# Optimization experiments

Hardware: AMD Instinct MI355X
Metric: run time of the kernel (lower is better)

Reference implementation:

```python
import jax, jax.numpy as jnp
import numpy as np

MEM, KD, VD, H, TEMP = 4096, 512, 512, 8, 1.0
B, N, BW = 4, 1024, 1024


def setup_inputs() -> dict:
    key = jax.random.key(0)
    ks = jax.random.split(key, 9)
    s = 0.02
    return {
        "queries": jax.random.normal(ks[0], (B, N, KD), jnp.float32),
        "write_keys": jax.random.normal(ks[1], (BW, KD), jnp.float32),
        "write_values": jax.random.normal(ks[2], (BW, VD), jnp.float32),
        "mem_keys": jax.random.normal(ks[3], (MEM, KD), jnp.float32),
        "mem_values": jax.random.normal(ks[4], (MEM, VD), jnp.float32),
        "Wq": jax.random.normal(ks[5], (KD, KD * H), jnp.float32) * s,
        "bq": jnp.zeros((KD * H,), jnp.float32),
        "Wvp": jax.random.normal(ks[6], (H * VD, VD), jnp.float32) * s,
        "bvp": jnp.zeros((VD,), jnp.float32),
        "Wg": jax.random.normal(ks[7], (KD + VD, KD), jnp.float32) * s,
        "bg": jnp.zeros((KD,), jnp.float32),
    }


def _read(queries, mem_keys, mem_values, Wq, bq, Wvp, bvp):
    b, n, _ = queries.shape
    q = queries @ Wq + bq                       # [b, n, H*KD]
    q = q.reshape(b, n, H, KD).transpose(0, 2, 1, 3)  # [b, h, n, d]
    # keys/values are shared across batch & heads: contract directly, no repeat
    scores = jnp.einsum('bhnd,md->bhnm', q, mem_keys) / (KD ** 0.5) / TEMP
    attn = jax.nn.softmax(scores, axis=-1)
    rv = jnp.einsum('bhnm,md->bhnd', attn, mem_values)  # [b, h, n, VD]
    rv = rv.transpose(0, 2, 1, 3).reshape(b, n, H * VD)
    return rv @ Wvp + bvp                        # [b, n, VD]


def _write(write_keys, write_values, mem_keys, mem_values, Wg, bg):
    eps = 1e-8
    kn = write_keys / jnp.maximum(jnp.linalg.norm(write_keys, axis=-1, keepdims=True), eps)
    mn = mem_keys / jnp.maximum(jnp.linalg.norm(mem_keys, axis=-1, keepdims=True), eps)
    idx = jnp.argmax(kn @ mn.T, axis=1)          # [BW] fixed against original keys

    def step(carry, inp):
        K, V = carry
        k, v, i = inp
        combined = jnp.concatenate([k, V[i]], axis=-1)   # reads current values
        gate = jax.nn.sigmoid(combined @ Wg + bg)        # [KD]
        K = K.at[i].set(gate * k + (1.0 - gate) * K[i])
        V = V.at[i].set(gate * v + (1.0 - gate) * V[i])
        return (K, V), None

    (nk, nv), _ = jax.lax.scan(step, (mem_keys, mem_values), (write_keys, write_values, idx))
    return nk, nv


def reference(queries, write_keys, write_values, mem_keys, mem_values, Wq, bq, Wvp, bvp, Wg, bg):
    read_out = _read(queries, mem_keys, mem_values, Wq, bq, Wvp, bvp)
    new_keys, new_values = _write(write_keys, write_values, mem_keys, mem_values, Wg, bg)
    return read_out, new_keys, new_values
```

## Files before the change

### kernel.cpp

```cpp
#include <hip/hip_runtime.h>
#include <cstdint>
#include <cstddef>

typedef __attribute__((ext_vector_type(8))) short short8;
typedef __attribute__((ext_vector_type(4))) float f32x4;
typedef unsigned char u8;
typedef unsigned short u16;
typedef unsigned int u32;
typedef unsigned long long u64;

__device__ __forceinline__ u16 f2bf(float f) {
    u32 u = __float_as_uint(f);
    u = (u + 0x7FFFu + ((u >> 16) & 1u)) >> 16;
    return (u16)u;
}
__device__ __forceinline__ float bf2f(u16 h) {
    u32 u = ((u32)h) << 16;
    return __uint_as_float(u);
}
__device__ __forceinline__ u8 f2fp8(float f) {
    return (u8)(__builtin_amdgcn_cvt_pk_fp8_f32(f, f, 0, false) & 0xFF);
}

__global__ void cast_bf16_kernel(const float* __restrict__ src, u16* __restrict__ dst) {
    int i = blockIdx.x * 256 + threadIdx.x;
    float4 v = *((const float4*)src + i);
    ushort4 r;
    r.x = f2bf(v.x); r.y = f2bf(v.y); r.z = f2bf(v.z); r.w = f2bf(v.w);
    *((ushort4*)dst + i) = r;
}

__global__ void split_bf16_kernel(const float* __restrict__ src,
                                  u16* __restrict__ hi, u16* __restrict__ lo) {
    int i = blockIdx.x * 256 + threadIdx.x;
    float4 v = *((const float4*)src + i);
    ushort4 h, l;
    h.x = f2bf(v.x); l.x = f2bf(v.x - bf2f(h.x));
    h.y = f2bf(v.y); l.y = f2bf(v.y - bf2f(h.y));
    h.z = f2bf(v.z); l.z = f2bf(v.z - bf2f(h.z));
    h.w = f2bf(v.w); l.w = f2bf(v.w - bf2f(h.w));
    *((ushort4*)hi + i) = h;
    *((ushort4*)lo + i) = l;
}

__global__ void cast_transpose_kernel(const float* __restrict__ src, u16* __restrict__ dst,
                                      int R, int C) {
    __shared__ float tile[32][33];
    int tx = threadIdx.x & 31, ty = threadIdx.x >> 5;
    int c0 = blockIdx.x * 32, r0 = blockIdx.y * 32;
#pragma unroll
    for (int j = 0; j < 4; j++)
        tile[ty + 8 * j][tx] = src[(size_t)(r0 + ty + 8 * j) * C + c0 + tx];
    __syncthreads();
#pragma unroll
    for (int j = 0; j < 4; j++)
        dst[(size_t)(c0 + ty + 8 * j) * R + r0 + tx] = f2bf(tile[tx][ty + 8 * j]);
}

__global__ void cast_transpose_fp8_kernel(const float* __restrict__ src, u8* __restrict__ dst,
                                          int R, int C) {
    __shared__ float tile[32][33];
    int tx = threadIdx.x & 31, ty = threadIdx.x >> 5;
    int c0 = blockIdx.x * 32, r0 = blockIdx.y * 32;
#pragma unroll
    for (int j = 0; j < 4; j++)
        tile[ty + 8 * j][tx] = src[(size_t)(r0 + ty + 8 * j) * C + c0 + tx];
    __syncthreads();
#pragma unroll
    for (int j = 0; j < 4; j++)
        dst[(size_t)(c0 + ty + 8 * j) * R + r0 + tx] = f2fp8(tile[tx][ty + 8 * j]);
}

__global__ __launch_bounds__(256) void key_prep_kernel(const float* __restrict__ mk,
                                                       u16* __restrict__ mn_hi,
                                                       u16* __restrict__ mn_lo,
                                                       u16* __restrict__ Kb) {
    int row = blockIdx.x, tid = threadIdx.x;
    const float* src = mk + (size_t)row * 512;
    float x0 = src[tid], x1 = src[tid + 256];
    float ss = x0 * x0 + x1 * x1;
#pragma unroll
    for (int m = 1; m < 64; m <<= 1) ss += __shfl_xor(ss, m);
    __shared__ float sred[4];
    if ((tid & 63) == 0) sred[tid >> 6] = ss;
    __syncthreads();
    float tot = sred[0] + sred[1] + sred[2] + sred[3];
    float inv = 1.0f / fmaxf(sqrtf(tot), 1e-8f);
    float n0 = x0 * inv, n1 = x1 * inv;
    u16 h0 = f2bf(n0), h1 = f2bf(n1);
    mn_hi[(size_t)row * 512 + tid] = h0;
    mn_hi[(size_t)row * 512 + tid + 256] = h1;
    mn_lo[(size_t)row * 512 + tid] = f2bf(n0 - bf2f(h0));
    mn_lo[(size_t)row * 512 + tid + 256] = f2bf(n1 - bf2f(h1));
    Kb[(size_t)row * 512 + tid] = f2bf(x0);
    Kb[(size_t)row * 512 + tid + 256] = f2bf(x1);
}

template <int BN, int EPI>
__global__ __launch_bounds__(256, 2) void gemm_bt_kernel(const u16* __restrict__ A,
                                                         const u16* __restrict__ Bt,
                                                         const float* __restrict__ bias,
                                                         void* __restrict__ Cout,
                                                         int M, int N, int K) {
    constexpr int NT = BN / 32;
    __shared__ __align__(16) u16 A_lds[128 * 40];
    __shared__ __align__(16) u16 B_lds[BN * 40];
    int tid = threadIdx.x;
    int w = tid >> 6, lane = tid & 63, l15 = lane & 15, quad = lane >> 4;
    int wm = w >> 1, wn = w & 1;
    int n0 = blockIdx.x * BN, m0 = blockIdx.y * 128;

    f32x4 acc[4][NT];
#pragma unroll
    for (int i = 0; i < 4; i++)
#pragma unroll
        for (int j = 0; j < NT; j++) acc[i][j] = (f32x4)(0.0f);

    for (int kt = 0; kt < K; kt += 32) {
        __syncthreads();
#pragma unroll
        for (int i = 0; i < 2; i++) {
            int c = i * 256 + tid;
            int r = c >> 2, col = c & 3;
            *(uint4*)&A_lds[r * 40 + col * 8] =
                *(const uint4*)&A[(size_t)(m0 + r) * K + kt + col * 8];
        }
#pragma unroll
        for (int i = 0; i < BN / 64; i++) {
            int c = i * 256 + tid;
            int r = c >> 2, col = c & 3;
            *(uint4*)&B_lds[r * 40 + col * 8] =
                *(const uint4*)&Bt[(size_t)(n0 + r) * K + kt + col * 8];
        }
        __syncthreads();
        short8 af[4], bf[NT];
#pragma unroll
        for (int mt = 0; mt < 4; mt++)
            af[mt] = *(const short8*)&A_lds[(wm * 64 + mt * 16 + l15) * 40 + quad * 8];
#pragma unroll
        for (int nt = 0; nt < NT; nt++)
            bf[nt] = *(const short8*)&B_lds[(wn * (BN / 2) + nt * 16 + l15) * 40 + quad * 8];
#pragma unroll
        for (int mt = 0; mt < 4; mt++)
#pragma unroll
            for (int nt = 0; nt < NT; nt++)
                acc[mt][nt] = __builtin_amdgcn_mfma_f32_16x16x32_bf16(af[mt], bf[nt], acc[mt][nt], 0, 0, 0);
    }

#pragma unroll
    for (int nt = 0; nt < NT; nt++) {
        int col = n0 + wn * (BN / 2) + nt * 16 + l15;
        float bs = bias[col];
#pragma unroll
        for (int mt = 0; mt < 4; mt++) {
            int row = m0 + wm * 64 + mt * 16 + quad * 4;
#pragma unroll
            for (int r = 0; r < 4; r++) {
                float v = acc[mt][nt][r] + bs;
                if (EPI == 0) {
                    ((float*)Cout)[(size_t)(row + r) * N + col] = v;
                } else {
                    int rr = row + r;
                    int bi = rr >> 10, ni = rr & 1023;
                    int h = col >> 9, d = col & 511;
                    ((u16*)Cout)[(((size_t)((bi * 8 + h)) * 1024 + ni)) * 512 + d] = f2bf(v);
                }
            }
        }
    }
}

__global__ __launch_bounds__(256, 2) void s_exp_gemm_kernel(const u16* __restrict__ A,
                                                            const u16* __restrict__ Bt,
                                                            u8* __restrict__ P,
                                                            float* __restrict__ denom) {
    __shared__ __align__(16) u16 A_lds[128 * 40];
    __shared__ __align__(16) u16 B_lds[128 * 40];
    int tid = threadIdx.x;
    int w = tid >> 6, lane = tid & 63, l15 = lane & 15, quad = lane >> 4;
    int wm = w >> 1, wn = w & 1;
    int n0 = blockIdx.x * 128, m0 = blockIdx.y * 128;

    f32x4 acc[4][4];
#pragma unroll
    for (int i = 0; i < 4; i++)
#pragma unroll
        for (int j = 0; j < 4; j++) acc[i][j] = (f32x4)(0.0f);

    for (int kt = 0; kt < 512; kt += 32) {
        __syncthreads();
#pragma unroll
        for (int i = 0; i < 2; i++) {
            int c = i * 256 + tid;
            int r = c >> 2, col = c & 3;
            *(uint4*)&A_lds[r * 40 + col * 8] =
                *(const uint4*)&A[(size_t)(m0 + r) * 512 + kt + col * 8];
            *(uint4*)&B_lds[r * 40 + col * 8] =
                *(const uint4*)&Bt[(size_t)(n0 + r) * 512 + kt + col * 8];
        }
        __syncthreads();
        short8 af[4], bf[4];
#pragma unroll
        for (int mt = 0; mt < 4; mt++)
            af[mt] = *(const short8*)&A_lds[(wm * 64 + mt * 16 + l15) * 40 + quad * 8];
#pragma unroll
        for (int nt = 0; nt < 4; nt++)
            bf[nt] = *(const short8*)&B_lds[(wn * 64 + nt * 16 + l15) * 40 + quad * 8];
#pragma unroll
        for (int mt = 0; mt < 4; mt++)
#pragma unroll
            for (int nt = 0; nt < 4; nt++)
                acc[mt][nt] = __builtin_amdgcn_mfma_f32_16x16x32_bf16(af[mt], bf[nt], acc[mt][nt], 0, 0, 0);
    }

    const float sc = 0.06375871826463886f;
#pragma unroll
    for (int mt = 0; mt < 4; mt++) {
#pragma unroll
        for (int r = 0; r < 4; r++) {
            int row = m0 + wm * 64 + mt * 16 + quad * 4 + r;
            float rs = 0.f;
#pragma unroll
            for (int nt = 0; nt < 4; nt++) {
                float p = exp2f(acc[mt][nt][r] * sc);
                rs += p;
                float pnb = __shfl_xor(p, 1);
                float plo = (l15 & 1) ? pnb : p;
                float phi = (l15 & 1) ? p : pnb;
                u32 pk2 = (u32)__builtin_amdgcn_cvt_pk_fp8_f32(plo, phi, 0, false) & 0xFFFFu;
                u32 oth = __shfl_xor(pk2, 2);
                u32 dw = (l15 & 2) ? (oth | (pk2 << 16)) : (pk2 | (oth << 16));
                if ((l15 & 3) == 0) {
                    int col = n0 + wn * 64 + nt * 16 + l15;
                    *(u32*)&P[(size_t)row * 4096 + col] = dw;
                }
            }
            rs += __shfl_xor(rs, 1); rs += __shfl_xor(rs, 2);
            rs += __shfl_xor(rs, 4); rs += __shfl_xor(rs, 8);
            if (l15 == 0) atomicAdd(&denom[row], rs);
        }
    }
}

__global__ __launch_bounds__(256, 2) void pv_gemm_kernel(const u8* __restrict__ A,
                                                         const u8* __restrict__ Bt,
                                                         const float* __restrict__ denom,
                                                         u16* __restrict__ rv,
                                                         int bh0) {
    __shared__ __align__(16) u8 A_lds[128 * 72];
    __shared__ __align__(16) u8 B_lds[128 * 72];
    int tid = threadIdx.x;
    int w = tid >> 6, lane = tid & 63, l15 = lane & 15, quad = lane >> 4;
    int wm = w >> 1, wn = w & 1;
    int m0 = blockIdx.x * 128, n0 = blockIdx.y * 128;

    f32x4 acc[4][4];
#pragma unroll
    for (int i = 0; i < 4; i++)
#pragma unroll
        for (int j = 0; j < 4; j++) acc[i][j] = (f32x4)(0.0f);

    for (int kt = 0; kt < 4096; kt += 64) {
        __syncthreads();
#pragma unroll
        for (int i = 0; i < 2; i++) {
            int c = i * 256 + tid;
            int r = c >> 2, seg = c & 3;
            *(uint4*)&A_lds[r * 72 + seg * 16] =
                *(const uint4*)&A[(size_t)(m0 + r) * 4096 + kt + seg * 16];
            *(uint4*)&B_lds[r * 72 + seg * 16] =
                *(const uint4*)&Bt[(size_t)(n0 + r) * 4096 + kt + seg * 16];
        }
        __syncthreads();
#pragma unroll
        for (int ks = 0; ks < 2; ks++) {
            long af[4], bf[4];
#pragma unroll
            for (int mt = 0; mt < 4; mt++)
                af[mt] = *(const long*)&A_lds[(wm * 64 + mt * 16 + l15) * 72 + ks * 32 + quad * 8];
#pragma unroll
            for (int nt = 0; nt < 4; nt++)
                bf[nt] = *(const long*)&B_lds[(wn * 64 + nt * 16 + l15) * 72 + ks * 32 + quad * 8];
#pragma unroll
            for (int mt = 0; mt < 4; mt++)
#pragma unroll
                for (int nt = 0; nt < 4; nt++)
                    acc[mt][nt] = __builtin_amdgcn_mfma_f32_16x16x32_fp8_fp8(af[mt], bf[nt], acc[mt][nt], 0, 0, 0);
        }
    }

#pragma unroll
    for (int mt = 0; mt < 4; mt++) {
#pragma unroll
        for (int r = 0; r < 4; r++) {
            int lr = m0 + wm * 64 + mt * 16 + quad * 4 + r;
            int gr = bh0 * 1024 + lr;
            float inv = 1.0f / denom[lr];
            int b = gr >> 13, h = (gr >> 10) & 7, n = gr & 1023;
            size_t base = ((size_t)(b * 1024 + n)) * 4096 + h * 512;
#pragma unroll
            for (int nt = 0; nt < 4; nt++) {
                int col = n0 + wn * 64 + nt * 16 + l15;
                float o = acc[mt][nt][r] * inv;
                float onb = __shfl_xor(o, 1);
                u16 blo = f2bf((l15 & 1) ? onb : o);
                u16 bhi = f2bf((l15 & 1) ? o : onb);
                u32 dw = (u32)blo | ((u32)bhi << 16);
                if (!(l15 & 1)) *(u32*)&rv[base + col] = dw;
            }
        }
    }
}

__global__ __launch_bounds__(256, 2) void sims_mfma_kernel(const u16* __restrict__ Ah,
                                                           const u16* __restrict__ Al,
                                                           const u16* __restrict__ Bh,
                                                           const u16* __restrict__ Bl,
                                                           u64* __restrict__ amax) {
    __shared__ __align__(16) u16 Ah_lds[128 * 40];
    __shared__ __align__(16) u16 Al_lds[128 * 40];
    __shared__ __align__(16) u16 Bh_lds[128 * 40];
    __shared__ __align__(16) u16 Bl_lds[128 * 40];
    int tid = threadIdx.x;
    int w = tid >> 6, lane = tid & 63, l15 = lane & 15, quad = lane >> 4;
    int wm = w >> 1, wn = w & 1;
    int n0 = blockIdx.x * 128, m0 = blockIdx.y * 128;

    f32x4 acc[4][4];
#pragma unroll
    for (int i = 0; i < 4; i++)
#pragma unroll
        for (int j = 0; j < 4; j++) acc[i][j] = (f32x4)(0.0f);

    for (int kt = 0; kt < 512; kt += 32) {
        __syncthreads();
#pragma unroll
        for (int i = 0; i < 2; i++) {
            int c = i * 256 + tid;
            int r = c >> 2, col = c & 3;
            size_t ga = (size_t)(m0 + r) * 512 + kt + col * 8;
            size_t gb = (size_t)(n0 + r) * 512 + kt + col * 8;
            *(uint4*)&Ah_lds[r * 40 + col * 8] = *(const uint4*)&Ah[ga];
            *(uint4*)&Al_lds[r * 40 + col * 8] = *(const uint4*)&Al[ga];
            *(uint4*)&Bh_lds[r * 40 + col * 8] = *(const uint4*)&Bh[gb];
            *(uint4*)&Bl_lds[r * 40 + col * 8] = *(const uint4*)&Bl[gb];
        }
        __syncthreads();
        short8 afh[4], afl[4], bfh[4], bfl[4];
#pragma unroll
        for (int mt = 0; mt < 4; mt++) {
            int off = (wm * 64 + mt * 16 + l15) * 40 + quad * 8;
            afh[mt] = *(const short8*)&Ah_lds[off];
            afl[mt] = *(const short8*)&Al_lds[off];
        }
#pragma unroll
        for (int nt = 0; nt < 4; nt++) {
            int off = (wn * 64 + nt * 16 + l15) * 40 + quad * 8;
            bfh[nt] = *(const short8*)&Bh_lds[off];
            bfl[nt] = *(const short8*)&Bl_lds[off];
        }
#pragma unroll
        for (int mt = 0; mt < 4; mt++)
#pragma unroll
            for (int nt = 0; nt < 4; nt++) {
                acc[mt][nt] = __builtin_amdgcn_mfma_f32_16x16x32_bf16(afh[mt], bfh[nt], acc[mt][nt], 0, 0, 0);
                acc[mt][nt] = __builtin_amdgcn_mfma_f32_16x16x32_bf16(afh[mt], bfl[nt], acc[mt][nt], 0, 0, 0);
                acc[mt][nt] = __builtin_amdgcn_mfma_f32_16x16x32_bf16(afl[mt], bfh[nt], acc[mt][nt], 0, 0, 0);
            }
    }

#pragma unroll
    for (int mt = 0; mt < 4; mt++) {
#pragma unroll
        for (int r = 0; r < 4; r++) {
            int row = m0 + wm * 64 + mt * 16 + quad * 4 + r;
            u64 best = 0;
#pragma unroll
            for (int nt = 0; nt < 4; nt++) {
                int col = n0 + wn * 64 + nt * 16 + l15;
                u32 bb = __float_as_uint(acc[mt][nt][r]);
                bb = (bb & 0x80000000u) ? ~bb : (bb | 0x80000000u);
                u64 key = ((u64)bb << 32) | (u32)(4095 - col);
                best = best > key ? best : key;
            }
            u64 o;
            o = __shfl_xor(best, 1); best = best > o ? best : o;
            o = __shfl_xor(best, 2); best = best > o ? best : o;
            o = __shfl_xor(best, 4); best = best > o ? best : o;
            o = __shfl_xor(best, 8); best = best > o ? best : o;
            if (l15 == 0) atomicMax(&amax[row], best);
        }
    }
}

__global__ __launch_bounds__(64) void chains_build_kernel(const u64* __restrict__ amax,
                                                          int* __restrict__ idx,
                                                          int* __restrict__ nxt,
                                                          int* __restrict__ heads,
                                                          int* __restrict__ count) {
    __shared__ int sidx[1024];
    int tid = threadIdx.x;
    for (int j = tid; j < 1024; j += 64)
        sidx[j] = 4095 - (int)(u32)(amax[j] & 0xFFFFFFFFull);
    __syncthreads();
    int i = blockIdx.x * 64 + tid;
    int my = sidx[i];
    idx[i] = my;
    int nx = -1;
    for (int j = i + 1; j < 1024; j++)
        if (sidx[j] == my) { nx = j; break; }
    nxt[i] = nx;
    bool head = true;
    for (int j = 0; j < i; j++)
        if (sidx[j] == my) { head = false; break; }
    if (head) {
        int p = atomicAdd(count, 1);
        heads[p] = i;
    }
}

__global__ __launch_bounds__(256) void g1_gemm_kernel(const float* __restrict__ wk,
                                                      const float* __restrict__ Wg,
                                                      const float* __restrict__ bg,
                                                      float* __restrict__ G1) {
    __shared__ float wkl[8][512];
    int tid = threadIdx.x;
    int i0 = blockIdx.x * 8;
    for (int i = tid; i < 8 * 512; i += 256) wkl[i >> 9][i & 511] = wk[(size_t)i0 * 512 + i];
    __syncthreads();
    float a0[8], a1[8];
#pragma unroll
    for (int i = 0; i < 8; i++) { a0[i] = 0.f; a1[i] = 0.f; }
    for (int c = 0; c < 512; c++) {
        float w0 = Wg[(size_t)c * 512 + tid];
        float w1 = Wg[(size_t)c * 512 + tid + 256];
#pragma unroll
        for (int ii = 0; ii < 8; ii++) {
            float s = wkl[ii][c];
            a0[ii] += s * w0; a1[ii] += s * w1;
        }
    }
    float b0 = bg[tid], b1 = bg[tid + 256];
#pragma unroll
    for (int ii = 0; ii < 8; ii++) {
        G1[(size_t)(i0 + ii) * 512 + tid] = a0[ii] + b0;
        G1[(size_t)(i0 + ii) * 512 + tid + 256] = a1[ii] + b1;
    }
}

__global__ __launch_bounds__(256) void chain_apply_kernel(const int* __restrict__ heads,
                                                          const int* __restrict__ count,
                                                          const int* __restrict__ idx,
                                                          const int* __restrict__ nxt,
                                                          const float* __restrict__ G1,
                                                          const float* __restrict__ Wg,
                                                          const float* __restrict__ wk,
                                                          const float* __restrict__ wv,
                                                          const float* __restrict__ mk,
                                                          const float* __restrict__ mv,
                                                          float* __restrict__ outK,
                                                          float* __restrict__ outV) {
    int b = blockIdx.x;
    if (b >= *count) return;
    int i = heads[b];
    int s = idx[i];
    int tid = threadIdx.x;
    __shared__ float V[512];
    V[tid] = mv[(size_t)s * 512 + tid];
    V[tid + 256] = mv[(size_t)s * 512 + tid + 256];
    float k0 = mk[(size_t)s * 512 + tid], k1 = mk[(size_t)s * 512 + tid + 256];
    __syncthreads();
    while (i >= 0) {
        float a0 = G1[(size_t)i * 512 + tid], a1 = G1[(size_t)i * 512 + tid + 256];
        for (int c = 0; c < 512; c++) {
            float vc = V[c];
            a0 += vc * Wg[(size_t)(512 + c) * 512 + tid];
            a1 += vc * Wg[(size_t)(512 + c) * 512 + tid + 256];
        }
        float g0 = 1.f / (1.f + __expf(-a0));
        float g1 = 1.f / (1.f + __expf(-a1));
        __syncthreads();
        k0 = g0 * wk[(size_t)i * 512 + tid] + (1.f - g0) * k0;
        k1 = g1 * wk[(size_t)i * 512 + tid + 256] + (1.f - g1) * k1;
        V[tid] = g0 * wv[(size_t)i * 512 + tid] + (1.f - g0) * V[tid];
        V[tid + 256] = g1 * wv[(size_t)i * 512 + tid + 256] + (1.f - g1) * V[tid + 256];
        __syncthreads();
        i = nxt[i];
    }
    outK[(size_t)s * 512 + tid] = k0;
    outK[(size_t)s * 512 + tid + 256] = k1;
    outV[(size_t)s * 512 + tid] = V[tid];
    outV[(size_t)s * 512 + tid + 256] = V[tid + 256];
}

extern "C" void kernel_launch(void* const* d_in, const int* in_sizes, int n_in,
                              void* d_out, int out_size, void* d_ws, size_t ws_size,
                              hipStream_t stream) {
    const float* queries = (const float*)d_in[0];
    const float* wkeys   = (const float*)d_in[1];
    const float* wvals   = (const float*)d_in[2];
    const float* mkeys   = (const float*)d_in[3];
    const float* mvals   = (const float*)d_in[4];
    const float* Wq      = (const float*)d_in[5];
    const float* bq      = (const float*)d_in[6];
    const float* Wvp     = (const float*)d_in[7];
    const float* bvp     = (const float*)d_in[8];
    const float* Wg      = (const float*)d_in[9];
    const float* bg      = (const float*)d_in[10];

    float* out_read = (float*)d_out;
    float* out_k = out_read + (size_t)4 * 1024 * 512;
    float* out_v = out_k + (size_t)4096 * 512;

    char* ws = (char*)d_ws;
    const size_t MB = 1024 * 1024;
    u16* Qbf  = (u16*)(ws);
    u16* WqT  = (u16*)(ws + 4 * MB);
    u16* Qatt = (u16*)(ws + 8 * MB);
    u16* Kb   = (u16*)(ws + 40 * MB);
    u8*  Vt8  = (u8*)(ws + 44 * MB);
    u16* rv   = (u16*)(ws + 48 * MB);
    u16* WvpT = (u16*)(ws + 80 * MB);
    u16* mn_hi = (u16*)(ws + 84 * MB);
    u16* mn_lo = (u16*)(ws + 88 * MB);
    float* G1  = (float*)(ws + 92 * MB);
    u16* wk_hi = (u16*)(ws + 94 * MB);
    u16* wk_lo = (u16*)(ws + 95 * MB);
    u64* amax   = (u64*)(ws);
    int* count  = (int*)(ws + 8192);
    int* idx    = (int*)(ws + 8192 + 256);
    int* nxt    = (int*)(ws + 8192 + 256 + 4096);
    int* heads  = (int*)(ws + 8192 + 256 + 8192);
    float* denom = (float*)(ws + 32 * 1024);
    u8* P = (u8*)(ws + 84 * MB);
    (void)in_sizes; (void)n_in; (void)out_size;

    size_t avail = (ws_size > 84 * MB) ? ws_size - 84 * MB : 0;
    int G = 2;
    for (int g = 32; g >= 2; g >>= 1)
        if ((size_t)g * 4 * MB <= avail) { G = g; break; }

    hipMemcpyAsync(out_k, mkeys, (size_t)4096 * 512 * 4, hipMemcpyDeviceToDevice, stream);
    hipMemcpyAsync(out_v, mvals, (size_t)4096 * 512 * 4, hipMemcpyDeviceToDevice, stream);

    cast_bf16_kernel<<<2048, 256, 0, stream>>>(queries, Qbf);
    cast_transpose_kernel<<<dim3(4096 / 32, 512 / 32), 256, 0, stream>>>(Wq, WqT, 512, 4096);
    cast_transpose_kernel<<<dim3(512 / 32, 4096 / 32), 256, 0, stream>>>(Wvp, WvpT, 4096, 512);
    cast_transpose_fp8_kernel<<<dim3(512 / 32, 4096 / 32), 256, 0, stream>>>(mvals, Vt8, 4096, 512);
    key_prep_kernel<<<4096, 256, 0, stream>>>(mkeys, mn_hi, mn_lo, Kb);
    split_bf16_kernel<<<512, 256, 0, stream>>>(wkeys, wk_hi, wk_lo);

    gemm_bt_kernel<128, 1><<<dim3(32, 32), 256, 0, stream>>>(Qbf, WqT, bq, (void*)Qatt, 4096, 4096, 512);

    hipMemsetAsync(ws, 0, 8192 + 256, stream);
    hipMemsetAsync(denom, 0, 32768 * 4, stream);
    sims_mfma_kernel<<<dim3(32, 8), 256, 0, stream>>>(wk_hi, wk_lo, mn_hi, mn_lo, amax);
    chains_build_kernel<<<16, 64, 0, stream>>>(amax, idx, nxt, heads, count);
    g1_gemm_kernel<<<128, 256, 0, stream>>>(wkeys, Wg, bg, G1);
    chain_apply_kernel<<<1024, 256, 0, stream>>>(heads, count, idx, nxt, G1, Wg,
                                                 wkeys, wvals, mkeys, mvals, out_k, out_v);

    for (int bh0 = 0; bh0 < 32; bh0 += G) {
        const u16* Achunk = Qatt + (size_t)bh0 * 1024 * 512;
        float* dchunk = denom + bh0 * 1024;
        s_exp_gemm_kernel<<<dim3(32, G * 8), 256, 0, stream>>>(Achunk, Kb, P, dchunk);
        pv_gemm_kernel<<<dim3(G * 8, 4), 256, 0, stream>>>(P, Vt8, dchunk, rv, bh0);
    }

    gemm_bt_kernel<64, 0><<<dim3(8, 32), 256, 0, stream>>>(rv, WvpT, bvp, (void*)out_read, 4096, 512, 4096);
}
```

Before: 825.7 us.

## Use direct global-to-LDS loads with XOR-swizzled unpadded tiles in GEMM kernels

Replaces register-staged global loads followed by LDS stores with global_load_lds direct transfers in all four MFMA GEMM kernels. Because direct LDS loads write contiguous 16-byte chunks per lane, the padded row stride is dropped and an XOR swizzle on the chunk index is applied when loading and when reading fragments, to avoid bank conflicts. This is meant to cut VGPR pressure and instruction count in the load phase. The loops stay single-buffered, so load latency still is not overlapped, and the swizzle has to match the fragment read pattern exactly.

```diff
diff --git a/kernel.cpp b/kernel.cpp
--- a/kernel.cpp
+++ b/kernel.cpp
@@ -20,6 +20,11 @@
 }
 __device__ __forceinline__ u8 f2fp8(float f) {
     return (u8)(__builtin_amdgcn_cvt_pk_fp8_f32(f, f, 0, false) & 0xFF);
+}
+
+__device__ __forceinline__ void gl_lds16(const void* g, void* l) {
+    __builtin_amdgcn_global_load_lds((const __attribute__((address_space(1))) void*)g,
+                                     (__attribute__((address_space(3))) void*)l, 16, 0, 0);
 }
 
 __global__ void cast_bf16_kernel(const float* __restrict__ src, u16* __restrict__ dst) {
@@ -103,12 +108,13 @@
                                                          void* __restrict__ Cout,
                                                          int M, int N, int K) {
     constexpr int NT = BN / 32;
-    __shared__ __align__(16) u16 A_lds[128 * 40];
-    __shared__ __align__(16) u16 B_lds[BN * 40];
+    __shared__ __align__(16) u16 A_lds[128 * 32];
+    __shared__ __align__(16) u16 B_lds[BN * 32];
     int tid = threadIdx.x;
     int w = tid >> 6, lane = tid & 63, l15 = lane & 15, quad = lane >> 4;
     int wm = w >> 1, wn = w & 1;
     int n0 = blockIdx.x * BN, m0 = blockIdx.y * 128;
+    int sa = (l15 >> 1) & 3;
 
     f32x4 acc[4][NT];
 #pragma unroll
@@ -121,25 +127,23 @@
 #pragma unroll
         for (int i = 0; i < 2; i++) {
             int c = i * 256 + tid;
-            int r = c >> 2, col = c & 3;
-            *(uint4*)&A_lds[r * 40 + col * 8] =
-                *(const uint4*)&A[(size_t)(m0 + r) * K + kt + col * 8];
+            int r = c >> 2, s = (c & 3) ^ ((r >> 1) & 3);
+            gl_lds16(&A[(size_t)(m0 + r) * K + kt + s * 8], &A_lds[c * 8]);
         }
 #pragma unroll
         for (int i = 0; i < BN / 64; i++) {
             int c = i * 256 + tid;
-            int r = c >> 2, col = c & 3;
-            *(uint4*)&B_lds[r * 40 + col * 8] =
-                *(const uint4*)&Bt[(size_t)(n0 + r) * K + kt + col * 8];
+            int r = c >> 2, s = (c & 3) ^ ((r >> 1) & 3);
+            gl_lds16(&Bt[(size_t)(n0 + r) * K + kt + s * 8], &B_lds[c * 8]);
         }
         __syncthreads();
         short8 af[4], bf[NT];
 #pragma unroll
         for (int mt = 0; mt < 4; mt++)
-            af[mt] = *(const short8*)&A_lds[(wm * 64 + mt * 16 + l15) * 40 + quad * 8];
+            af[mt] = *(const short8*)&A_lds[(wm * 64 + mt * 16 + l15) * 32 + (quad ^ sa) * 8];
 #pragma unroll
         for (int nt = 0; nt < NT; nt++)
-            bf[nt] = *(const short8*)&B_lds[(wn * (BN / 2) + nt * 16 + l15) * 40 + quad * 8];
+            bf[nt] = *(const short8*)&B_lds[(wn * (BN / 2) + nt * 16 + l15) * 32 + (quad ^ sa) * 8];
 #pragma unroll
         for (int mt = 0; mt < 4; mt++)
 #pragma unroll
@@ -174,12 +178,13 @@
                                                             const u16* __restrict__ Bt,
                                                             u8* __restrict__ P,
                                                             float* __restrict__ denom) {
-    __shared__ __align__(16) u16 A_lds[128 * 40];
-    __shared__ __align__(16) u16 B_lds[128 * 40];
+    __shared__ __align__(16) u16 A_lds[128 * 32];
+    __shared__ __align__(16) u16 B_lds[128 * 32];
     int tid = threadIdx.x;
     int w = tid >> 6, lane = tid & 63, l15 = lane & 15, quad = lane >> 4;
     int wm = w >> 1, wn = w & 1;
     int n0 = blockIdx.x * 128, m0 = blockIdx.y * 128;
+    int sa = (l15 >> 1) & 3;
 
     f32x4 acc[4][4];
 #pragma unroll
@@ -192,20 +197,18 @@
 #pragma unroll
         for (int i = 0; i < 2; i++) {
             int c = i * 256 + tid;
-            int r = c >> 2, col = c & 3;
-            *(uint4*)&A_lds[r * 40 + col * 8] =
-                *(const uint4*)&A[(size_t)(m0 + r) * 512 + kt + col * 8];
-            *(uint4*)&B_lds[r * 40 + col * 8] =
-                *(const uint4*)&Bt[(size_t)(n0 + r) * 512 + kt + col * 8];
+            int r = c >> 2, s = (c & 3) ^ ((r >> 1) & 3);
+            gl_lds16(&A[(size_t)(m0 + r) * 512 + kt + s * 8], &A_lds[c * 8]);
+            gl_lds16(&Bt[(size_t)(n0 + r) * 512 + kt + s * 8], &B_lds[c * 8]);
         }
         __syncthreads();
         short8 af[4], bf[4];
 #pragma unroll
         for (int mt = 0; mt < 4; mt++)
-            af[mt] = *(const short8*)&A_lds[(wm * 64 + mt * 16 + l15) * 40 + quad * 8];
+            af[mt] = *(const short8*)&A_lds[(wm * 64 + mt * 16 + l15) * 32 + (quad ^ sa) * 8];
 #pragma unroll
         for (int nt = 0; nt < 4; nt++)
-            bf[nt] = *(const short8*)&B_lds[(wn * 64 + nt * 16 + l15) * 40 + quad * 8];
+            bf[nt] = *(const short8*)&B_lds[(wn * 64 + nt * 16 + l15) * 32 + (quad ^ sa) * 8];
 #pragma unroll
         for (int mt = 0; mt < 4; mt++)
 #pragma unroll
@@ -247,12 +250,13 @@
                                                          const float* __restrict__ denom,
                                                          u16* __restrict__ rv,
                                                          int bh0) {
-    __shared__ __align__(16) u8 A_lds[128 * 72];
-    __shared__ __align__(16) u8 B_lds[128 * 72];
+    __shared__ __align__(16) u8 A_lds[128 * 64];
+    __shared__ __align__(16) u8 B_lds[128 * 64];
     int tid = threadIdx.x;
     int w = tid >> 6, lane = tid & 63, l15 = lane & 15, quad = lane >> 4;
     int wm = w >> 1, wn = w & 1;
     int m0 = blockIdx.x * 128, n0 = blockIdx.y * 128;
+    int sa = (l15 >> 1) & 3;
 
     f32x4 acc[4][4];
 #pragma unroll
@@ -265,22 +269,24 @@
 #pragma unroll
         for (int i = 0; i < 2; i++) {
             int c = i * 256 + tid;
-            int r = c >> 2, seg = c & 3;
-            *(uint4*)&A_lds[r * 72 + seg * 16] =
-                *(const uint4*)&A[(size_t)(m0 + r) * 4096 + kt + seg * 16];
-            *(uint4*)&B_lds[r * 72 + seg * 16] =
-                *(const uint4*)&Bt[(size_t)(n0 + r) * 4096 + kt + seg * 16];
+            int r = c >> 2, s = (c & 3) ^ ((r >> 1) & 3);
+            gl_lds16(&A[(size_t)(m0 + r) * 4096 + kt + s * 16], &A_lds[c * 16]);
+            gl_lds16(&Bt[(size_t)(n0 + r) * 4096 + kt + s * 16], &B_lds[c * 16]);
         }
         __syncthreads();
 #pragma unroll
         for (int ks = 0; ks < 2; ks++) {
             long af[4], bf[4];
 #pragma unroll
-            for (int mt = 0; mt < 4; mt++)
-                af[mt] = *(const long*)&A_lds[(wm * 64 + mt * 16 + l15) * 72 + ks * 32 + quad * 8];
-#pragma unroll
-            for (int nt = 0; nt < 4; nt++)
-                bf[nt] = *(const long*)&B_lds[(wn * 64 + nt * 16 + l15) * 72 + ks * 32 + quad * 8];
+            for (int mt = 0; mt < 4; mt++) {
+                int row = wm * 64 + mt * 16 + l15;
+                af[mt] = *(const long*)&A_lds[row * 64 + (((ks * 2 + (quad >> 1)) ^ sa) * 16) + (quad & 1) * 8];
+            }
+#pragma unroll
+            for (int nt = 0; nt < 4; nt++) {
+                int row = wn * 64 + nt * 16 + l15;
+                bf[nt] = *(const long*)&B_lds[row * 64 + (((ks * 2 + (quad >> 1)) ^ sa) * 16) + (quad & 1) * 8];
+            }
 #pragma unroll
             for (int mt = 0; mt < 4; mt++)
 #pragma unroll
@@ -317,14 +323,15 @@
                                                            const u16* __restrict__ Bh,
                                                            const u16* __restrict__ Bl,
                                                            u64* __restrict__ amax) {
-    __shared__ __align__(16) u16 Ah_lds[128 * 40];
-    __shared__ __align__(16) u16 Al_lds[128 * 40];
-    __shared__ __align__(16) u16 Bh_lds[128 * 40];
-    __shared__ __align__(16) u16 Bl_lds[128 * 40];
+    __shared__ __align__(16) u16 Ah_lds[128 * 32];
+    __shared__ __align__(16) u16 Al_lds[128 * 32];
+    __shared__ __align__(16) u16 Bh_lds[128 * 32];
+    __shared__ __align__(16) u16 Bl_lds[128 * 32];
     int tid = threadIdx.x;
     int w = tid >> 6, lane = tid & 63, l15 = lane & 15, quad = lane >> 4;
     int wm = w >> 1, wn = w & 1;
     int n0 = blockIdx.x * 128, m0 = blockIdx.y * 128;
+    int sa = (l15 >> 1) & 3;
 
     f32x4 acc[4][4];
 #pragma unroll
@@ -337,25 +344,25 @@
 #pragma unroll
         for (int i = 0; i < 2; i++) {
             int c = i * 256 + tid;
-            int r = c >> 2, col = c & 3;
-            size_t ga = (size_t)(m0 + r) * 512 + kt + col * 8;
-            size_t gb = (size_t)(n0 + r) * 512 + kt + col * 8;
-            *(uint4*)&Ah_lds[r * 40 + col * 8] = *(const uint4*)&Ah[ga];
-            *(uint4*)&Al_lds[r * 40 + col * 8] = *(const uint4*)&Al[ga];
-            *(uint4*)&Bh_lds[r * 40 + col * 8] = *(const uint4*)&Bh[gb];
-            *(uint4*)&Bl_lds[r * 40 + col * 8] = *(const uint4*)&Bl[gb];
+            int r = c >> 2, s = (c & 3) ^ ((r >> 1) & 3);
+            size_t ga = (size_t)(m0 + r) * 512 + kt + s * 8;
+            size_t gb = (size_t)(n0 + r) * 512 + kt + s * 8;
+            gl_lds16(&Ah[ga], &Ah_lds[c * 8]);
+            gl_lds16(&Al[ga], &Al_lds[c * 8]);
+            gl_lds16(&Bh[gb], &Bh_lds[c * 8]);
+            gl_lds16(&Bl[gb], &Bl_lds[c * 8]);
         }
         __syncthreads();
         short8 afh[4], afl[4], bfh[4], bfl[4];
 #pragma unroll
         for (int mt = 0; mt < 4; mt++) {
-            int off = (wm * 64 + mt * 16 + l15) * 40 + quad * 8;
+            int off = (wm * 64 + mt * 16 + l15) * 32 + (quad ^ sa) * 8;
             afh[mt] = *(const short8*)&Ah_lds[off];
             afl[mt] = *(const short8*)&Al_lds[off];
         }
 #pragma unroll
         for (int nt = 0; nt < 4; nt++) {
-            int off = (wn * 64 + nt * 16 + l15) * 40 + quad * 8;
+            int off = (wn * 64 + nt * 16 + l15) * 32 + (quad ^ sa) * 8;
             bfh[nt] = *(const short8*)&Bh_lds[off];
             bfl[nt] = *(const short8*)&Bl_lds[off];
         }
```

After: 799.9 us. 1.03x faster.
